# Performance work log

Measured on AMD Instinct MI355X. Metric: run time of the kernel, lower is better.

Reference implementation:

```python
import jax, jax.numpy as jnp
import numpy as np

D_MODEL = 256
D_INNER = 512          # expand * d_model
HEADDIM = 64
NHEADS = D_INNER // HEADDIM   # 8
NGROUPS = 1
D_STATE = 64
D_IN_PROJ = 2 * D_INNER + 2 * NGROUPS * D_STATE + NHEADS   # 1160
CONV_DIM = D_INNER + 2 * NGROUPS * D_STATE                  # 640
LN_EPS = 1e-5


def setup_inputs() -> dict:
    key = jax.random.key(0)
    ks = jax.random.split(key, 16)
    s = 0.02
    # dt_bias init as in torch code
    dt = jnp.exp(jax.random.uniform(ks[10], (NHEADS,)) * (np.log(0.1) - np.log(0.001)) + np.log(0.001))
    dt = jnp.clip(dt, 1e-4)
    dt_bias = dt + jnp.log(-jnp.expm1(-dt))
    A_log = jnp.log(jax.random.uniform(ks[11], (NHEADS,), minval=1.0, maxval=16.0))
    return {
        "u": jax.random.normal(ks[0], (4, 8192, D_MODEL), dtype=jnp.float32),
        "H": 64,
        "W": 128,
        "W_in": jax.random.normal(ks[1], (D_IN_PROJ, D_MODEL), dtype=jnp.float32) * s,
        "W_stereo": jax.random.normal(ks[2], (D_IN_PROJ, D_INNER), dtype=jnp.float32) * s,
        "conv_l_w": jax.random.normal(ks[3], (CONV_DIM, 1, 3, 3), dtype=jnp.float32) * 0.1,
        "conv_l_b": jax.random.normal(ks[4], (CONV_DIM,), dtype=jnp.float32) * 0.01,
        "conv_r_w": jax.random.normal(ks[5], (CONV_DIM, 1, 3, 3), dtype=jnp.float32) * 0.1,
        "conv_r_b": jax.random.normal(ks[6], (CONV_DIM,), dtype=jnp.float32) * 0.01,
        "conv_w": jax.random.normal(ks[7], (CONV_DIM, 1, 3, 3), dtype=jnp.float32) * 0.1,
        "conv_b": jax.random.normal(ks[8], (CONV_DIM,), dtype=jnp.float32) * 0.01,
        "dt_bias": dt_bias,
        "A_log": A_log,
        "D_l": jnp.ones((NHEADS,), dtype=jnp.float32),
        "D_r": jnp.ones((NHEADS,), dtype=jnp.float32),
        "D": jnp.ones((NHEADS,), dtype=jnp.float32),
        "ln_g": jnp.ones((D_INNER,), dtype=jnp.float32),
        "ln_b": jnp.zeros((D_INNER,), dtype=jnp.float32),
        "W_out": jax.random.normal(ks[9], (D_MODEL, D_INNER), dtype=jnp.float32) * s,
    }


def _dwconv(x, w, b):
    # x: (B, C, H, W); depthwise 3x3 conv, SAME padding ((d_conv-1)//2 = 1)
    y = jax.lax.conv_general_dilated(
        x, w, window_strides=(1, 1), padding='SAME',
        dimension_numbers=('NCHW', 'OIHW', 'NCHW'),
        feature_group_count=CONV_DIM)
    return y + b[None, :, None, None]


def _layernorm(x, g, b):
    mu = x.mean(-1, keepdims=True)
    var = x.var(-1, keepdims=True)
    return (x - mu) / jnp.sqrt(var + LN_EPS) * g + b


def _lin_attn(x, dt, A, Bm, Cm, Dp):
    # x: (b, l, d_inner), dt: (b, l, h), Bm/Cm: (b, l, d_state); ngroups == 1
    b, l, _ = x.shape
    xh = x.reshape(b, l, NHEADS, HEADDIM)              # V: (b, l, h, p)
    dA = -(dt[..., None] * A[None, None, :, None])     # ssd_positve_dA -> -dt*A, (b,l,h,1)
    KV = jnp.einsum('bls,blhp->bhsp', Bm, xh * dA)     # K^T @ V_scaled
    y = jnp.einsum('bls,bhsp->blhp', Cm, KV)           # Q @ KV
    y = y + xh * Dp[None, None, :, None]               # skip D
    return y.reshape(b, l, D_INNER)


def reference(u, H, W, W_in, W_stereo, conv_l_w, conv_l_b, conv_r_w, conv_r_b,
              conv_w, conv_b, dt_bias, A_log, D_l, D_r, D, ln_g, ln_b, W_out):
    batch, seqlen, _ = u.shape
    half = batch // 2
    silu = jax.nn.silu
    A = -jnp.exp(A_log)

    zxbcdt = u @ W_in.T                                             # (b, l, 1160)
    z, xBC, dt = jnp.split(zxbcdt, [D_INNER, D_INNER + CONV_DIM], axis=-1)
    dt = jax.nn.softplus(dt + dt_bias)                              # (b, l, h)

    xBC = xBC.reshape(batch, H, W, CONV_DIM).transpose(0, 3, 1, 2)  # NCHW
    xBC1 = silu(_dwconv(xBC[:half], conv_l_w, conv_l_b)).transpose(0, 2, 3, 1).reshape(half, H * W, CONV_DIM)
    xBC2 = silu(_dwconv(xBC[half:], conv_r_w, conv_r_b)).transpose(0, 2, 3, 1).reshape(half, H * W, CONV_DIM)

    x1, B1, C1 = jnp.split(xBC1, [D_INNER, D_INNER + NGROUPS * D_STATE], axis=-1)
    x2, B2, C2 = jnp.split(xBC2, [D_INNER, D_INNER + NGROUPS * D_STATE], axis=-1)
    dt1, dt2 = dt[:half], dt[half:]

    y1 = _layernorm(_lin_attn(x1, dt1, A, B1, C1, D_l), ln_g, ln_b)
    y2 = _layernorm(_lin_attn(x2, dt2, A, B2, C2, D_r), ln_g, ln_b)
    y = jnp.concatenate([y1, y2], axis=0) * z

    zxs = y @ W_stereo.T
    zs, xBCs, dts = jnp.split(zxs, [D_INNER, D_INNER + CONV_DIM], axis=-1)
    dts = jax.nn.softplus(dts + dt_bias)

    xBCs = xBCs.reshape(batch, H, W, CONV_DIM).transpose(0, 3, 1, 2)
    xBCs = silu(_dwconv(xBCs, conv_w, conv_b)).transpose(0, 2, 3, 1).reshape(batch, H * W, CONV_DIM)
    xs, Bs, Cs = jnp.split(xBCs, [D_INNER, D_INNER + NGROUPS * D_STATE], axis=-1)

    ys = _layernorm(_lin_attn(xs, dts, A, Bs, Cs, D), ln_g, ln_b) * zs
    return ys @ W_out.T
```

## Files before the change

### kernel.cpp

```cpp
#include <hip/hip_runtime.h>
#include <hip/hip_bf16.h>
#include <math.h>

#define NB    4
#define LSEQ  8192
#define HH    64
#define WW    128
#define DMODEL 256
#define DINNER 512
#define NH    8
#define DSTATE 64
#define DPROJ 1160
#define CONVD 640
#define MROWS (NB*LSEQ)
#define KVCH  32
#define CBLK  80

typedef unsigned short bf16_t;
typedef __attribute__((ext_vector_type(8))) unsigned short ushort8v;
typedef __attribute__((ext_vector_type(8))) short short8v;
typedef __attribute__((ext_vector_type(4))) float f32x4;

static __device__ __forceinline__ float bf2f(bf16_t u) {
    return __uint_as_float(((unsigned)u) << 16);
}
static __device__ __forceinline__ bf16_t f2bf(float f) {
    unsigned u = __float_as_uint(f);
    u += 0x7FFFu + ((u >> 16) & 1u);
    return (bf16_t)(u >> 16);
}

template <typename TC>
__global__ __launch_bounds__(512) void gemm_mfma_big(
    const bf16_t* __restrict__ A, int lda,
    const bf16_t* __restrict__ B, int ldb,
    TC* __restrict__ C, int ldc,
    int M, int N, int K)
{
    __shared__ __align__(16) bf16_t As[2][256 * 32];
    __shared__ __align__(16) bf16_t Bs[2][128 * 32];
    const int nwg = gridDim.x * gridDim.y;
    const int wg  = blockIdx.y * gridDim.x + blockIdx.x;
    const int swz = (wg & 7) * (nwg >> 3) + (wg >> 3);
    const int bx  = swz % gridDim.x;
    const int by  = swz / gridDim.x;

    const int tid = threadIdx.x;
    const int m0 = by * 256;
    const int n0 = bx * 128;
    const int w    = tid >> 6;
    const int lane = tid & 63;
    const int wrow = w >> 1;
    const int wcol = w & 1;
    const int fr = lane & 15;
    const int kq = lane >> 4;

    f32x4 acc[4][4];
    #pragma unroll
    for (int i = 0; i < 4; ++i)
        #pragma unroll
        for (int j = 0; j < 4; ++j) acc[i][j] = (f32x4){0.f, 0.f, 0.f, 0.f};

    int arow[2], acol[2];
    #pragma unroll
    for (int i = 0; i < 2; ++i) {
        const int L = i * 512 + tid;
        arow[i] = ((L >> 8) << 6) + (((L >> 6) & 3) << 4) + ((L >> 2) & 15);
        acol[i] = (L & 3) * 8;
    }
    const int Lb = tid;
    const int brow = ((Lb >> 8) << 6) + (((Lb >> 6) & 3) << 4) + ((Lb >> 2) & 15);
    const int bcol = (Lb & 3) * 8;

#define STAGE_BIG(buf, k0)                                                     \
    {                                                                          \
        _Pragma("unroll")                                                      \
        for (int i = 0; i < 2; ++i) {                                          \
            const size_t ga = (size_t)(m0 + arow[i]) * lda + (k0) + acol[i];   \
            __builtin_amdgcn_global_load_lds(                                  \
                (const __attribute__((address_space(1))) void*)(A + ga),       \
                (__attribute__((address_space(3))) void*)(&As[buf][(i * 512 + tid) * 8]), 16, 0, 0); \
        }                                                                      \
        const size_t gb = (size_t)(n0 + brow) * ldb + (k0) + bcol;             \
        __builtin_amdgcn_global_load_lds(                                      \
            (const __attribute__((address_space(1))) void*)(B + gb),           \
            (__attribute__((address_space(3))) void*)(&Bs[buf][tid * 8]), 16, 0, 0); \
    }

    const int nt = K >> 5;
    STAGE_BIG(0, 0);
    __syncthreads();

    const int abase = wrow * 2048 + (fr * 4 + kq) * 8;
    const int bbase = wcol * 2048 + (fr * 4 + kq) * 8;

    int cur = 0;
    for (int t = 0; t < nt; ++t) {
        if (t + 1 < nt) STAGE_BIG(cur ^ 1, (t + 1) * 32);

        short8v a_frag[4], b_frag[4];
        #pragma unroll
        for (int m = 0; m < 4; ++m)
            a_frag[m] = *(const short8v*)&As[cur][abase + m * 512];
        #pragma unroll
        for (int n = 0; n < 4; ++n)
            b_frag[n] = *(const short8v*)&Bs[cur][bbase + n * 512];
        #pragma unroll
        for (int m = 0; m < 4; ++m)
            #pragma unroll
            for (int n = 0; n < 4; ++n)
                acc[m][n] = __builtin_amdgcn_mfma_f32_16x16x32_bf16(
                    a_frag[m], b_frag[n], acc[m][n], 0, 0, 0);

        __syncthreads();
        cur ^= 1;
    }
#undef STAGE_BIG

    #pragma unroll
    for (int mi = 0; mi < 4; ++mi) {
        #pragma unroll
        for (int ni = 0; ni < 4; ++ni) {
            const int col = n0 + wcol * 64 + ni * 16 + fr;
            if (col < N) {
                #pragma unroll
                for (int q = 0; q < 4; ++q) {
                    const int row = m0 + wrow * 64 + mi * 16 + kq * 4 + q;
                    if constexpr (sizeof(TC) == 2)
                        C[(size_t)row * ldc + col] = f2bf(acc[mi][ni][q]);
                    else
                        C[(size_t)row * ldc + col] = acc[mi][ni][q];
                }
            }
        }
    }
}

template <typename TC>
__global__ __launch_bounds__(256) void gemm_mfma_bt(
    const bf16_t* __restrict__ A, int lda, size_t sAb,
    const bf16_t* __restrict__ B, int ldb, size_t sBb,
    TC* __restrict__ C, int ldc, size_t sCb,
    int M, int N, int K)
{
    __shared__ __align__(16) bf16_t As[128 * 32];
    __shared__ __align__(16) bf16_t Bs[128 * 32];
    const bf16_t* Ab = A + blockIdx.z * sAb;
    const bf16_t* Bb = B + blockIdx.z * sBb;
    TC*            Cb = C + blockIdx.z * sCb;
    const int tid = threadIdx.x;
    const int m0 = blockIdx.y * 128;
    const int n0 = blockIdx.x * 128;
    const int wid = tid >> 6;
    const int lane = tid & 63;
    const int wr = (wid >> 1) * 64;
    const int wc = (wid & 1) * 64;
    const int fr = lane & 15;
    const int fk = (lane >> 4) * 8;

    f32x4 acc[4][4];
    #pragma unroll
    for (int i = 0; i < 4; ++i)
        #pragma unroll
        for (int j = 0; j < 4; ++j) acc[i][j] = (f32x4){0.f, 0.f, 0.f, 0.f};

    const int srow = tid >> 2;
    const int scol = (tid & 3) * 8;
    const bf16_t* gA = Ab + (size_t)(m0 + srow) * lda + scol;
    const bf16_t* gB = Bb + (size_t)(n0 + srow) * ldb + scol;
    bf16_t* lA = As + tid * 8;
    bf16_t* lB = Bs + tid * 8;

    for (int k0 = 0; k0 < K; k0 += 32) {
        __builtin_amdgcn_global_load_lds(
            (const __attribute__((address_space(1))) void*)(gA + k0),
            (__attribute__((address_space(3))) void*)lA, 16, 0, 0);
        __builtin_amdgcn_global_load_lds(
            (const __attribute__((address_space(1))) void*)(gA + (size_t)64 * lda + k0),
            (__attribute__((address_space(3))) void*)(lA + 2048), 16, 0, 0);
        __builtin_amdgcn_global_load_lds(
            (const __attribute__((address_space(1))) void*)(gB + k0),
            (__attribute__((address_space(3))) void*)lB, 16, 0, 0);
        __builtin_amdgcn_global_load_lds(
            (const __attribute__((address_space(1))) void*)(gB + (size_t)64 * ldb + k0),
            (__attribute__((address_space(3))) void*)(lB + 2048), 16, 0, 0);
        __syncthreads();

        short8v a_frag[4], b_frag[4];
        #pragma unroll
        for (int m = 0; m < 4; ++m)
            a_frag[m] = *(const short8v*)&As[(wr + m * 16 + fr) * 32 + fk];
        #pragma unroll
        for (int n = 0; n < 4; ++n)
            b_frag[n] = *(const short8v*)&Bs[(wc + n * 16 + fr) * 32 + fk];
        #pragma unroll
        for (int m = 0; m < 4; ++m)
            #pragma unroll
            for (int n = 0; n < 4; ++n)
                acc[m][n] = __builtin_amdgcn_mfma_f32_16x16x32_bf16(
                    a_frag[m], b_frag[n], acc[m][n], 0, 0, 0);
        __syncthreads();
    }

    #pragma unroll
    for (int mi = 0; mi < 4; ++mi) {
        #pragma unroll
        for (int ni = 0; ni < 4; ++ni) {
            const int col = n0 + wc + ni * 16 + fr;
            if (col < N) {
                #pragma unroll
                for (int q = 0; q < 4; ++q) {
                    const int row = m0 + wr + mi * 16 + (lane >> 4) * 4 + q;
                    if constexpr (sizeof(TC) == 2)
                        Cb[(size_t)row * ldc + col] = f2bf(acc[mi][ni][q]);
                    else
                        Cb[(size_t)row * ldc + col] = acc[mi][ni][q];
                }
            }
        }
    }
}

__global__ __launch_bounds__(256) void cvt_bf16_kernel(
    const float* __restrict__ in, bf16_t* __restrict__ out, int n)
{
    const int base = (blockIdx.x * 256 + threadIdx.x) * 4;
    if (base >= n) return;
    float4 v = *(const float4*)&in[base];
    ushort4 o;
    o.x = f2bf(v.x); o.y = f2bf(v.y); o.z = f2bf(v.z); o.w = f2bf(v.w);
    *(ushort4*)&out[base] = o;
}

__global__ __launch_bounds__(256) void wpad_kernel(
    const float* __restrict__ W, bf16_t* __restrict__ Wp,
    int N, int Npad, int K)
{
    const int i = blockIdx.x * 256 + threadIdx.x;
    if (i >= Npad * K) return;
    const int r = i / K, k = i - r * K;
    Wp[i] = (r < N) ? f2bf(W[(size_t)r * K + k]) : (bf16_t)0;
}

__global__ __launch_bounds__(256) void dt_kernel(
    const bf16_t* __restrict__ zx, const float* __restrict__ dt_bias,
    float* __restrict__ dtbuf)
{
    const int idx = blockIdx.x * 256 + threadIdx.x;
    const int h = idx & 7;
    const int row = idx >> 3;
    const float v = bf2f(zx[(size_t)row * DPROJ + (DINNER + CONVD) + h]) + dt_bias[h];
    const float sp = (v > 0.f) ? (v + log1pf(expf(-v))) : log1pf(expf(v));
    dtbuf[idx] = sp;
}

__global__ __launch_bounds__(256) void conv_silu_kernel(
    const bf16_t* __restrict__ zx,
    const float* __restrict__ wA, const float* __restrict__ bA,
    const float* __restrict__ wB, const float* __restrict__ bB,
    bf16_t* __restrict__ out)
{
    const int idx = blockIdx.x * 256 + threadIdx.x;
    const int cb = idx % CBLK;
    const int pc = idx / CBLK;
    const int c0 = cb * 8;
    const int ww = pc & (WW - 1);
    const int h4 = (pc >> 7) & 15;
    const int b  = pc >> 11;
    const int hbase = h4 * 4;
    const float* wp = (b < 2) ? wA : wB;
    const float* bp = (b < 2) ? bA : bB;

    float w[72];
    const float4* wsrc = (const float4*)(wp + c0 * 9);
    #pragma unroll
    for (int i = 0; i < 18; ++i) ((float4*)w)[i] = wsrc[i];

    float acc[4][8];
    {
        float4 bv0 = *(const float4*)(bp + c0);
        float4 bv1 = *(const float4*)(bp + c0 + 4);
        #pragma unroll
        for (int o = 0; o < 4; ++o) {
            acc[o][0] = bv0.x; acc[o][1] = bv0.y; acc[o][2] = bv0.z; acc[o][3] = bv0.w;
            acc[o][4] = bv1.x; acc[o][5] = bv1.y; acc[o][6] = bv1.z; acc[o][7] = bv1.w;
        }
    }

    const bf16_t* base = zx + (size_t)b * LSEQ * DPROJ + DINNER + c0;
    #pragma unroll
    for (int ri = 0; ri < 6; ++ri) {
        const int hi = hbase + ri - 1;
        const bool hok = (unsigned)hi < (unsigned)HH;
        float cur[3][8];
        #pragma unroll
        for (int kj = 0; kj < 3; ++kj) {
            const int wi = ww + kj - 1;
            if (hok && (unsigned)wi < (unsigned)WW) {
                const ushort8v v = *(const ushort8v*)(base + (size_t)(hi * WW + wi) * DPROJ);
                #pragma unroll
                for (int q = 0; q < 8; ++q) cur[kj][q] = bf2f(v[q]);
            } else {
                #pragma unroll
                for (int q = 0; q < 8; ++q) cur[kj][q] = 0.f;
            }
        }
        #pragma unroll
        for (int o = 0; o < 4; ++o) {
            const int ki = ri - o;
            if (ki >= 0 && ki < 3) {
                #pragma unroll
                for (int kj = 0; kj < 3; ++kj)
                    #pragma unroll
                    for (int q = 0; q < 8; ++q)
                        acc[o][q] += cur[kj][q] * w[q * 9 + ki * 3 + kj];
            }
        }
    }

    #pragma unroll
    for (int o = 0; o < 4; ++o) {
        const int t = b * LSEQ + (hbase + o) * WW + ww;
        ushort8v ov;
        #pragma unroll
        for (int q = 0; q < 8; ++q) {
            const float s = acc[o][q] / (1.f + expf(-acc[o][q]));
            ov[q] = f2bf(s);
        }
        *(ushort8v*)(out + (size_t)t * CONVD + c0) = ov;
    }
}

__global__ __launch_bounds__(128) void kv_part_kernel(
    const bf16_t* __restrict__ xconv, const float* __restrict__ dtbuf,
    const float* __restrict__ A_log, float* __restrict__ KVp)
{
    const int h = blockIdx.y, b = blockIdx.z, chunk = blockIdx.x;
    const int tid = threadIdx.x;
    const int w = tid >> 6, lane = tid & 63;
    __shared__ float lds[2 * 4352];
    float* Bt = lds + w * 4352;
    float* Xt = Bt + 2176;
    const float eA = expf(A_log[h]);
    const int s4  = (lane & 15) * 4;
    const int p16 = (lane >> 4) * 16;
    const int r    = lane & 31;
    const int part = lane >> 5;

    float acc[4][16];
    #pragma unroll
    for (int i = 0; i < 4; ++i)
        #pragma unroll
        for (int j = 0; j < 16; ++j) acc[i][j] = 0.f;

    const int l0 = b * LSEQ + chunk * 256;

    for (int t = 0; t < 8; t += 2) {
        const int row = l0 + (t + w) * 32 + r;
        const bf16_t* src = xconv + (size_t)row * CONVD + (part ? h * 64 : DINNER);
        const float scale = part ? dtbuf[row * NH + h] * eA : 1.f;
        float* dst = part ? &Xt[r * 68] : &Bt[r * 68];
        #pragma unroll
        for (int j = 0; j < 8; ++j) {
            ushort8v v = *(const ushort8v*)(src + j * 8);
            f32x4 lo = {bf2f(v[0]) * scale, bf2f(v[1]) * scale,
                        bf2f(v[2]) * scale, bf2f(v[3]) * scale};
            f32x4 hi = {bf2f(v[4]) * scale, bf2f(v[5]) * scale,
                        bf2f(v[6]) * scale, bf2f(v[7]) * scale};
            *(f32x4*)&dst[j * 8]     = lo;
            *(f32x4*)&dst[j * 8 + 4] = hi;
        }
        __syncthreads();
        #pragma unroll 4
        for (int rr = 0; rr < 32; ++rr) {
            const f32x4 bv = *(const f32x4*)&Bt[rr * 68 + s4];
            #pragma unroll
            for (int q = 0; q < 4; ++q) {
                const f32x4 xv = *(const f32x4*)&Xt[rr * 68 + p16 + q * 4];
                #pragma unroll
                for (int si = 0; si < 4; ++si)
                    #pragma unroll
                    for (int k = 0; k < 4; ++k)
                        acc[si][q * 4 + k] += bv[si] * xv[k];
            }
        }
        __syncthreads();
    }

    if (w == 0) {
        #pragma unroll
        for (int si = 0; si < 4; ++si)
            #pragma unroll
            for (int q = 0; q < 4; ++q)
                *(f32x4*)&lds[(s4 + si) * 68 + p16 + q * 4] =
                    (f32x4){acc[si][q*4], acc[si][q*4+1], acc[si][q*4+2], acc[si][q*4+3]};
    }
    __syncthreads();
    if (w == 1) {
        float* dst = KVp + ((size_t)chunk * (NB * NH) + (b * NH + h)) * 4096;
        #pragma unroll
        for (int si = 0; si < 4; ++si)
            #pragma unroll
            for (int q = 0; q < 4; ++q) {
                const f32x4 o = *(const f32x4*)&lds[(s4 + si) * 68 + p16 + q * 4];
                f32x4 v = {acc[si][q*4] + o[0], acc[si][q*4+1] + o[1],
                           acc[si][q*4+2] + o[2], acc[si][q*4+3] + o[3]};
                *(f32x4*)&dst[(s4 + si) * 64 + p16 + q * 4] = v;
            }
    }
}

__global__ __launch_bounds__(256) void kv_reduce_T_kernel(
    const float* __restrict__ KVp, bf16_t* __restrict__ KVT)
{
    const int idx = blockIdx.x * 256 + threadIdx.x;
    float s = 0.f;
    #pragma unroll
    for (int c = 0; c < KVCH; ++c) s += KVp[(size_t)c * 131072 + idx];
    const int bh = idx >> 12;
    const int ss = (idx >> 6) & 63;
    const int p  = idx & 63;
    KVT[((size_t)(bh * 64 + p)) * 64 + ss] = f2bf(s);
}

__global__ __launch_bounds__(256) void ln_gate_kernel(
    const bf16_t* __restrict__ Yattn, const bf16_t* __restrict__ xconv,
    const bf16_t* __restrict__ zx,
    const float* __restrict__ DA, const float* __restrict__ DB,
    const float* __restrict__ ln_g, const float* __restrict__ ln_b,
    bf16_t* __restrict__ ybuf)
{
    const int w = threadIdx.x >> 6, lane = threadIdx.x & 63;
    const int c0 = lane * 8;
    const int h = lane >> 3;
    float g[8], be[8];
    *(float4*)&g[0]  = *(const float4*)&ln_g[c0];
    *(float4*)&g[4]  = *(const float4*)&ln_g[c0 + 4];
    *(float4*)&be[0] = *(const float4*)&ln_b[c0];
    *(float4*)&be[4] = *(const float4*)&ln_b[c0 + 4];
    const int row0 = (blockIdx.x * 4 + w) * 4;

    for (int i = 0; i < 4; ++i) {
        const int row = row0 + i;
        const int b = row >> 13;
        const float Dv = (b < 2) ? DA[h] : DB[h];
        ushort8v yv = *(const ushort8v*)(Yattn + (size_t)row * DINNER + c0);
        ushort8v xv = *(const ushort8v*)(xconv + (size_t)row * CONVD + c0);
        float y[8];
        float s1 = 0.f, s2 = 0.f;
        #pragma unroll
        for (int q = 0; q < 8; ++q) {
            y[q] = bf2f(yv[q]) + bf2f(xv[q]) * Dv;
            s1 += y[q]; s2 += y[q] * y[q];
        }
        #pragma unroll
        for (int off = 32; off > 0; off >>= 1) {
            s1 += __shfl_xor(s1, off, 64);
            s2 += __shfl_xor(s2, off, 64);
        }
        const float mu = s1 * (1.f / 512.f);
        const float var = s2 * (1.f / 512.f) - mu * mu;
        const float rstd = rsqrtf(var + 1e-5f);
        ushort8v zv = *(const ushort8v*)(zx + (size_t)row * DPROJ + c0);
        ushort8v o;
        #pragma unroll
        for (int q = 0; q < 8; ++q)
            o[q] = f2bf(((y[q] - mu) * rstd * g[q] + be[q]) * bf2f(zv[q]));
        *(ushort8v*)(ybuf + (size_t)row * DINNER + c0) = o;
    }
}

extern "C" void kernel_launch(void* const* d_in, const int* in_sizes, int n_in,
                              void* d_out, int out_size, void* d_ws, size_t ws_size,
                              hipStream_t stream)
{
    const float* u        = (const float*)d_in[0];
    const float* W_in     = (const float*)d_in[3];
    const float* W_st     = (const float*)d_in[4];
    const float* conv_l_w = (const float*)d_in[5];
    const float* conv_l_b = (const float*)d_in[6];
    const float* conv_r_w = (const float*)d_in[7];
    const float* conv_r_b = (const float*)d_in[8];
    const float* conv_w   = (const float*)d_in[9];
    const float* conv_b   = (const float*)d_in[10];
    const float* dt_bias  = (const float*)d_in[11];
    const float* A_log    = (const float*)d_in[12];
    const float* D_l      = (const float*)d_in[13];
    const float* D_r      = (const float*)d_in[14];
    const float* Dp       = (const float*)d_in[15];
    const float* ln_g     = (const float*)d_in[16];
    const float* ln_b     = (const float*)d_in[17];
    const float* W_out    = (const float*)d_in[18];
    float* out = (float*)d_out;

    char* ws = (char*)d_ws;
    const size_t ZX_B    = (size_t)MROWS * DPROJ * 2;
    const size_t XCONV_B = (size_t)MROWS * CONVD * 2;
    const size_t YBUF_B  = (size_t)MROWS * DINNER * 2;
    const size_t DT_B    = (size_t)MROWS * NH * 4;
    const size_t KVT_B   = (size_t)NB * DINNER * 64 * 2;
    const size_t UBF_B   = (size_t)MROWS * DMODEL * 2;
    const size_t WIN_B   = (size_t)1280 * DMODEL * 2;
    const size_t WST_B   = (size_t)1280 * DINNER * 2;
    const size_t WOUT_B  = (size_t)256 * DINNER * 2;
    bf16_t* zx    = (bf16_t*)(ws);
    bf16_t* xconv = (bf16_t*)(ws + ZX_B);
    bf16_t* ybuf  = (bf16_t*)(ws + ZX_B + XCONV_B);
    float*  dtbuf = (float*) (ws + ZX_B + XCONV_B + YBUF_B);
    bf16_t* KVT   = (bf16_t*)(ws + ZX_B + XCONV_B + YBUF_B + DT_B);
    bf16_t* ubf   = (bf16_t*)(ws + ZX_B + XCONV_B + YBUF_B + DT_B + KVT_B);
    float*  KVp   = (float*) (ws + ZX_B + XCONV_B + YBUF_B + DT_B + KVT_B);
    bf16_t* WinP  = (bf16_t*)(ws + ZX_B + XCONV_B + YBUF_B + DT_B + KVT_B + UBF_B);
    bf16_t* WstP  = (bf16_t*)(ws + ZX_B + XCONV_B + YBUF_B + DT_B + KVT_B + UBF_B + WIN_B);
    bf16_t* WoutP = (bf16_t*)(ws + ZX_B + XCONV_B + YBUF_B + DT_B + KVT_B + UBF_B + WIN_B + WST_B);
    bf16_t* Yattn = (bf16_t*)(ws + ZX_B + XCONV_B + YBUF_B + DT_B + KVT_B + UBF_B + WIN_B + WST_B + WOUT_B);

    const dim3 gemmGridP(10, MROWS / 256);
    const dim3 gemmGridO(2,  MROWS / 256);
    const dim3 ymmGrid(4, LSEQ / 128, NB);
    const dim3 kvGrid(KVCH, NH, NB);
    const int convGrid = (MROWS / 4) * CBLK / 256;
    const int lnGrid = MROWS / 16;

    cvt_bf16_kernel<<<(MROWS * DMODEL / 4 + 255) / 256, 256, 0, stream>>>(u, ubf, MROWS * DMODEL);
    wpad_kernel<<<(1280 * DMODEL + 255) / 256, 256, 0, stream>>>(W_in, WinP, DPROJ, 1280, DMODEL);
    wpad_kernel<<<(1280 * DINNER + 255) / 256, 256, 0, stream>>>(W_st, WstP, DPROJ, 1280, DINNER);
    wpad_kernel<<<(256 * DINNER + 255) / 256, 256, 0, stream>>>(W_out, WoutP, DMODEL, 256, DINNER);

    gemm_mfma_big<bf16_t><<<gemmGridP, 512, 0, stream>>>(
        ubf, DMODEL, WinP, DMODEL, zx, DPROJ, MROWS, DPROJ, DMODEL);
    dt_kernel<<<(MROWS * NH) / 256, 256, 0, stream>>>(zx, dt_bias, dtbuf);
    conv_silu_kernel<<<convGrid, 256, 0, stream>>>(
        zx, conv_l_w, conv_l_b, conv_r_w, conv_r_b, xconv);
    kv_part_kernel<<<kvGrid, 128, 0, stream>>>(xconv, dtbuf, A_log, KVp);
    kv_reduce_T_kernel<<<131072 / 256, 256, 0, stream>>>(KVp, KVT);
    gemm_mfma_bt<bf16_t><<<ymmGrid, 256, 0, stream>>>(
        xconv + DINNER + DSTATE, CONVD, (size_t)LSEQ * CONVD,
        KVT, 64, (size_t)DINNER * 64,
        Yattn, DINNER, (size_t)LSEQ * DINNER, LSEQ, DINNER, 64);
    ln_gate_kernel<<<lnGrid, 256, 0, stream>>>(
        Yattn, xconv, zx, D_l, D_r, ln_g, ln_b, ybuf);

    gemm_mfma_big<bf16_t><<<gemmGridP, 512, 0, stream>>>(
        ybuf, DINNER, WstP, DINNER, zx, DPROJ, MROWS, DPROJ, DINNER);
    dt_kernel<<<(MROWS * NH) / 256, 256, 0, stream>>>(zx, dt_bias, dtbuf);
    conv_silu_kernel<<<convGrid, 256, 0, stream>>>(
        zx, conv_w, conv_b, conv_w, conv_b, xconv);
    kv_part_kernel<<<kvGrid, 128, 0, stream>>>(xconv, dtbuf, A_log, KVp);
    kv_reduce_T_kernel<<<131072 / 256, 256, 0, stream>>>(KVp, KVT);
    gemm_mfma_bt<bf16_t><<<ymmGrid, 256, 0, stream>>>(
        xconv + DINNER + DSTATE, CONVD, (size_t)LSEQ * CONVD,
        KVT, 64, (size_t)DINNER * 64,
        Yattn, DINNER, (size_t)LSEQ * DINNER, LSEQ, DINNER, 64);
    ln_gate_kernel<<<lnGrid, 256, 0, stream>>>(
        Yattn, xconv, zx, Dp, Dp, ln_g, ln_b, ybuf);

    gemm_mfma_big<float><<<gemmGridO, 512, 0, stream>>>(
        ybuf, DINNER, WoutP, DINNER, out, DMODEL, MROWS, DMODEL, DINNER);
}
```

Baseline: 387.2 us.

## Fuse dt softplus into kv_part and switch output projection to bt GEMM

Removes the standalone dt_kernel and computes the softplus of the dt projection plus bias inline in kv_part_kernel, reading zx directly. This drops two launches and the dtbuf round trip, but repeats the softplus across the 32 chunks' threads. It also swaps the final output GEMM from gemm_mfma_big (512 threads, 256-row tiles) to gemm_mfma_bt (256 threads, 128-row tiles), which changes tile shape and block count.

```diff
diff --git a/kernel.cpp b/kernel.cpp
--- a/kernel.cpp
+++ b/kernel.cpp
@@ -242,18 +242,6 @@
     Wp[i] = (r < N) ? f2bf(W[(size_t)r * K + k]) : (bf16_t)0;
 }
 
-__global__ __launch_bounds__(256) void dt_kernel(
-    const bf16_t* __restrict__ zx, const float* __restrict__ dt_bias,
-    float* __restrict__ dtbuf)
-{
-    const int idx = blockIdx.x * 256 + threadIdx.x;
-    const int h = idx & 7;
-    const int row = idx >> 3;
-    const float v = bf2f(zx[(size_t)row * DPROJ + (DINNER + CONVD) + h]) + dt_bias[h];
-    const float sp = (v > 0.f) ? (v + log1pf(expf(-v))) : log1pf(expf(v));
-    dtbuf[idx] = sp;
-}
-
 __global__ __launch_bounds__(256) void conv_silu_kernel(
     const bf16_t* __restrict__ zx,
     const float* __restrict__ wA, const float* __restrict__ bA,
@@ -332,7 +320,8 @@
 }
 
 __global__ __launch_bounds__(128) void kv_part_kernel(
-    const bf16_t* __restrict__ xconv, const float* __restrict__ dtbuf,
+    const bf16_t* __restrict__ xconv, const bf16_t* __restrict__ zx,
+    const float* __restrict__ dt_bias,
     const float* __restrict__ A_log, float* __restrict__ KVp)
 {
     const int h = blockIdx.y, b = blockIdx.z, chunk = blockIdx.x;
@@ -342,6 +331,7 @@
     float* Bt = lds + w * 4352;
     float* Xt = Bt + 2176;
     const float eA = expf(A_log[h]);
+    const float dtb = dt_bias[h];
     const int s4  = (lane & 15) * 4;
     const int p16 = (lane >> 4) * 16;
     const int r    = lane & 31;
@@ -358,7 +348,12 @@
     for (int t = 0; t < 8; t += 2) {
         const int row = l0 + (t + w) * 32 + r;
         const bf16_t* src = xconv + (size_t)row * CONVD + (part ? h * 64 : DINNER);
-        const float scale = part ? dtbuf[row * NH + h] * eA : 1.f;
+        float scale = 1.f;
+        if (part) {
+            const float v = bf2f(zx[(size_t)row * DPROJ + (DINNER + CONVD) + h]) + dtb;
+            const float sp = (v > 0.f) ? (v + log1pf(expf(-v))) : log1pf(expf(v));
+            scale = sp * eA;
+        }
         float* dst = part ? &Xt[r * 68] : &Bt[r * 68];
         #pragma unroll
         for (int j = 0; j < 8; ++j) {
@@ -506,7 +501,6 @@
     bf16_t* zx    = (bf16_t*)(ws);
     bf16_t* xconv = (bf16_t*)(ws + ZX_B);
     bf16_t* ybuf  = (bf16_t*)(ws + ZX_B + XCONV_B);
-    float*  dtbuf = (float*) (ws + ZX_B + XCONV_B + YBUF_B);
     bf16_t* KVT   = (bf16_t*)(ws + ZX_B + XCONV_B + YBUF_B + DT_B);
     bf16_t* ubf   = (bf16_t*)(ws + ZX_B + XCONV_B + YBUF_B + DT_B + KVT_B);
     float*  KVp   = (float*) (ws + ZX_B + XCONV_B + YBUF_B + DT_B + KVT_B);
@@ -516,7 +510,7 @@
     bf16_t* Yattn = (bf16_t*)(ws + ZX_B + XCONV_B + YBUF_B + DT_B + KVT_B + UBF_B + WIN_B + WST_B + WOUT_B);
 
     const dim3 gemmGridP(10, MROWS / 256);
-    const dim3 gemmGridO(2,  MROWS / 256);
+    const dim3 gemmGridO(2,  MROWS / 128, 1);
     const dim3 ymmGrid(4, LSEQ / 128, NB);
     const dim3 kvGrid(KVCH, NH, NB);
     const int convGrid = (MROWS / 4) * CBLK / 256;
@@ -529,10 +523,9 @@
 
     gemm_mfma_big<bf16_t><<<gemmGridP, 512, 0, stream>>>(
         ubf, DMODEL, WinP, DMODEL, zx, DPROJ, MROWS, DPROJ, DMODEL);
-    dt_kernel<<<(MROWS * NH) / 256, 256, 0, stream>>>(zx, dt_bias, dtbuf);
     conv_silu_kernel<<<convGrid, 256, 0, stream>>>(
         zx, conv_l_w, conv_l_b, conv_r_w, conv_r_b, xconv);
-    kv_part_kernel<<<kvGrid, 128, 0, stream>>>(xconv, dtbuf, A_log, KVp);
+    kv_part_kernel<<<kvGrid, 128, 0, stream>>>(xconv, zx, dt_bias, A_log, KVp);
     kv_reduce_T_kernel<<<131072 / 256, 256, 0, stream>>>(KVp, KVT);
     gemm_mfma_bt<bf16_t><<<ymmGrid, 256, 0, stream>>>(
         xconv + DINNER + DSTATE, CONVD, (size_t)LSEQ * CONVD,
@@ -543,10 +536,9 @@
 
     gemm_mfma_big<bf16_t><<<gemmGridP, 512, 0, stream>>>(
         ybuf, DINNER, WstP, DINNER, zx, DPROJ, MROWS, DPROJ, DINNER);
-    dt_kernel<<<(MROWS * NH) / 256, 256, 0, stream>>>(zx, dt_bias, dtbuf);
     conv_silu_kernel<<<convGrid, 256, 0, stream>>>(
         zx, conv_w, conv_b, conv_w, conv_b, xconv);
-    kv_part_kernel<<<kvGrid, 128, 0, stream>>>(xconv, dtbuf, A_log, KVp);
+    kv_part_kernel<<<kvGrid, 128, 0, stream>>>(xconv, zx, dt_bias, A_log, KVp);
     kv_reduce_T_kernel<<<131072 / 256, 256, 0, stream>>>(KVp, KVT);
     gemm_mfma_bt<bf16_t><<<ymmGrid, 256, 0, stream>>>(
         xconv + DINNER + DSTATE, CONVD, (size_t)LSEQ * CONVD,
@@ -555,6 +547,6 @@
     ln_gate_kernel<<<lnGrid, 256, 0, stream>>>(
         Yattn, xconv, zx, Dp, Dp, ln_g, ln_b, ybuf);
 
-    gemm_mfma_big<float><<<gemmGridO, 512, 0, stream>>>(
-        ybuf, DINNER, WoutP, DINNER, out, DMODEL, MROWS, DMODEL, DINNER);
-}
+    gemm_mfma_bt<float><<<gemmGridO, 256, 0, stream>>>(
+        ybuf, DINNER, 0, WoutP, DINNER, 0, out, DMODEL, 0, MROWS, DMODEL, DINNER);
+}
```

Measured after the change: 385.0 us (median of 2 runs). Within noise of the previous version (-0.6%).
